# Performance work log

Measured on AMD Instinct MI355X. Metric: run time of the kernel, lower is better.

The kernel has to match this reference:

```python
import jax, jax.numpy as jnp
import numpy as np

H = 16  # heads
EPS_LN = 1e-5

def _ln(x, g, b):
    m = jnp.mean(x, axis=-1, keepdims=True)
    v = jnp.mean((x - m) ** 2, axis=-1, keepdims=True)
    return (x - m) / jnp.sqrt(v + EPS_LN) * g + b

def setup_inputs() -> dict:
    key = jax.random.key(0)
    B, L, d, mlp = 4, 4096, 1024, 4096
    ks = jax.random.split(key, 12)
    s = 0.02
    inp = {
        'x':   jax.random.normal(ks[0], (B, L, d), jnp.float32),
        'Wq':  jax.random.normal(ks[1], (d, d), jnp.float32) * s,
        'bq':  jnp.zeros((d,), jnp.float32),
        'gq':  jnp.ones((d,), jnp.float32),
        'betaq': jnp.zeros((d,), jnp.float32),
        'Wk':  jax.random.normal(ks[2], (d, d), jnp.float32) * s,
        'bk':  jnp.zeros((d,), jnp.float32),
        'gk':  jnp.ones((d,), jnp.float32),
        'betak': jnp.zeros((d,), jnp.float32),
        'Wv':  jax.random.normal(ks[3], (d, d), jnp.float32) * s,
        'bv':  jnp.zeros((d,), jnp.float32),
        'gv':  jnp.ones((d,), jnp.float32),
        'betav': jnp.zeros((d,), jnp.float32),
        'Wfq': jax.random.normal(ks[4], (d, d), jnp.float32) * s,
        'bfq': jnp.zeros((d,), jnp.float32),
        'Wfk': jax.random.normal(ks[5], (d, d), jnp.float32) * s,
        'bfk': jnp.zeros((d,), jnp.float32),
        'ga':  jnp.ones((d,), jnp.float32),
        'ba':  jnp.zeros((d,), jnp.float32),
        'W1':  jax.random.normal(ks[6], (d, mlp), jnp.float32) * s,
        'b1':  jnp.zeros((mlp,), jnp.float32),
        'W2':  jax.random.normal(ks[7], (mlp, d), jnp.float32) * s,
        'b2':  jnp.zeros((d,), jnp.float32),
    }
    return inp

def _fwd(x, Wq, bq, gq, betaq, Wk, bk, gk, betak, Wv, bv, gv, betav,
         Wfq, bfq, Wfk, bfk, ga, ba, W1, b1, W2, b2):
    B, L, d = x.shape
    D = d // H
    # Q/K/V projections + LayerNorm (dropout is eval-mode identity)
    Q = _ln(x @ Wq + bq, gq, betaq)                      # [B,L,d]
    Kc = _ln(x @ Wk + bk, gk, betak)                     # [B,L,d]
    Vc = _ln(x @ Wv + bv, gv, betav)                     # [B,L,d]
    # prepend zero token to K and V (add_zero_token=True)
    z = jnp.zeros((B, 1, d), x.dtype)
    K = jnp.concatenate([z, Kc], axis=1)                 # [B,Lk,d], Lk=L+1
    V = jnp.concatenate([z, Vc], axis=1)
    # kernel feature maps: tanh(Linear(.)) + 1
    phi_Q = jnp.tanh(Q @ Wfq + bfq) + 1.0
    phi_K = jnp.tanh(K @ Wfk + bfk) + 1.0
    split = lambda t: t.reshape(B, t.shape[1], H, D).transpose(0, 2, 1, 3)
    Qh, Kh, Vh = split(Q), split(K), split(V)            # [B,H,L(,k),D]
    pQ, pK = split(phi_Q), split(phi_K)
    # probe-softmax gating of phi_K
    q_probe = jnp.mean(Qh, axis=2) / jnp.sqrt(jnp.asarray(D, x.dtype))  # [B,H,D]
    score = jax.nn.softmax(jnp.einsum('bhd,bhkd->bhk', q_probe, Kh), axis=-1)  # [B,H,Lk]
    pKw = pK * score[..., None]                          # [B,H,Lk,D]
    # linear-attention fast path
    KV = jnp.einsum('bhkd,bhke->bhde', pKw, Vh)          # [B,H,D,D]
    Ksum = jnp.sum(pKw, axis=2)                          # [B,H,D]
    num = jnp.einsum('bhqd,bhde->bhqe', pQ, KV)          # [B,H,L,D]
    den = jnp.einsum('bhqd,bhd->bhq', pQ, Ksum)[..., None] + 1e-6
    out = num / den                                      # [B,H,L,D]
    out = out.transpose(0, 2, 1, 3).reshape(B, L, d)     # merge heads
    a = _ln(out, ga, ba)                                 # attn_norm
    # Residual MLP: a + Linear2(GELU(Linear1(a)))  (exact erf GELU)
    h = a + (jax.nn.gelu(a @ W1 + b1, approximate=False) @ W2 + b2)
    return h + x                                         # outer residual

def reference(x, Wq, bq, gq, betaq, Wk, bk, gk, betak, Wv, bv, gv, betav,
              Wfq, bfq, Wfk, bfk, ga, ba, W1, b1, W2, b2):
    return _fwd(x, Wq, bq, gq, betaq, Wk, bk, gk, betak, Wv, bv, gv, betav,
                Wfq, bfq, Wfk, bfk, ga, ba, W1, b1, W2, b2)
```

## Files before the change

### kernel.cpp

```cpp
#include <hip/hip_runtime.h>
#include <cstddef>
#include <cstdint>

static constexpr int Bc   = 4;
static constexpr int Lq   = 4096;
static constexpr int Dm   = 1024;
static constexpr int Dmlp = 4096;
static constexpr int Mrows = Bc * Lq;
static constexpr int Lk1   = Lq + 1;

typedef unsigned short u16;
typedef __bf16 bf16_t;
typedef bf16_t bf16x8 __attribute__((ext_vector_type(8)));
typedef float  f32x4  __attribute__((ext_vector_type(4)));

__device__ __forceinline__ u16 f2b(float f) {
    uint32_t u = __builtin_bit_cast(uint32_t, f);
    return (u16)((u + 0x7FFFu + ((u >> 16) & 1u)) >> 16);
}
__device__ __forceinline__ float b2f(u16 h) {
    uint32_t u = ((uint32_t)h) << 16;
    return __builtin_bit_cast(float, u);
}

#define GLL16(gsrc, ldst) \
    __builtin_amdgcn_global_load_lds( \
        (const __attribute__((address_space(1))) void*)(gsrc), \
        (__attribute__((address_space(3))) void*)(ldst), 16, 0, 0)

__global__ __launch_bounds__(256)
void zero_kernel(float* __restrict__ p, int n) {
    const int i = blockIdx.x * 256 + threadIdx.x;
    if (i < n) p[i] = 0.0f;
}

__global__ __launch_bounds__(256)
void cvt_bf16_kernel(const float* __restrict__ in, u16* __restrict__ outp, int n) {
    for (int i = (blockIdx.x * 256 + threadIdx.x) * 4; i < n; i += gridDim.x * 256 * 4) {
        float4 v = *(const float4*)&in[i];
        ushort4 o = { f2b(v.x), f2b(v.y), f2b(v.z), f2b(v.w) };
        *(ushort4*)&outp[i] = o;
    }
}

__global__ __launch_bounds__(256)
void transpose_bf16_kernel(const float* __restrict__ in, u16* __restrict__ outp,
                           int R, int C) {
    __shared__ float tile[64][65];
    const int r0 = blockIdx.y * 64, c0 = blockIdx.x * 64;
    const int t = threadIdx.x;
    const int lr = t >> 2, lc0 = (t & 3) * 16;
    #pragma unroll
    for (int j = 0; j < 4; ++j) {
        float4 v = *(const float4*)&in[(size_t)(r0 + lr) * C + c0 + lc0 + j * 4];
        tile[lr][lc0 + j * 4 + 0] = v.x;
        tile[lr][lc0 + j * 4 + 1] = v.y;
        tile[lr][lc0 + j * 4 + 2] = v.z;
        tile[lr][lc0 + j * 4 + 3] = v.w;
    }
    __syncthreads();
    const int oc = t >> 2, rr0 = (t & 3) * 16;
    union { u16 u[16]; uint4 v[2]; } pk;
    #pragma unroll
    for (int j = 0; j < 16; ++j) pk.u[j] = f2b(tile[rr0 + j][oc]);
    u16* po = &outp[(size_t)(c0 + oc) * R + r0 + rr0];
    *(uint4*)&po[0] = pk.v[0];
    *(uint4*)&po[8] = pk.v[1];
}

__global__ __launch_bounds__(256)
void kvt_cvt_kernel(const float* __restrict__ KV, u16* __restrict__ KVT) {
    const int bh = blockIdx.x;
    __shared__ float t[64][65];
    const int tid = threadIdx.x;
    const int r = tid >> 2, c0 = (tid & 3) * 16;
    const float* src = &KV[(size_t)bh * 4096];
    #pragma unroll
    for (int j = 0; j < 4; ++j) {
        float4 v = *(const float4*)&src[r * 64 + c0 + j * 4];
        t[r][c0 + j * 4 + 0] = v.x;
        t[r][c0 + j * 4 + 1] = v.y;
        t[r][c0 + j * 4 + 2] = v.z;
        t[r][c0 + j * 4 + 3] = v.w;
    }
    __syncthreads();
    const int e = tid >> 2, d0 = (tid & 3) * 16;
    union { u16 u[16]; uint4 v[2]; } pk;
    #pragma unroll
    for (int j = 0; j < 16; ++j) pk.u[j] = f2b(t[d0 + j][e]);
    u16* po = &KVT[(size_t)bh * 4096 + e * 64 + d0];
    *(uint4*)&po[0] = pk.v[0];
    *(uint4*)&po[8] = pk.v[1];
}

template<int ACT, bool RES, bool ACCUM, bool BIAS, bool OBF16>
__global__ __launch_bounds__(512, 1)
void mfma_gemm256(const u16* __restrict__ A, int ldA,
                  const u16* __restrict__ Bt, int ldB,
                  const float* __restrict__ bias,
                  void* __restrict__ Cout,
                  const u16* __restrict__ res1, const float* __restrict__ res2,
                  int M, int N, int K) {
    __shared__ u16 ldsA[4][8192];
    __shared__ u16 ldsB[4][8192];
    const int tid = threadIdx.x;
    const int l   = tid & 63;
    const int w   = tid >> 6;
    const int wm  = w >> 2;
    const int wn  = w & 3;
    const int l16 = l & 15, l4 = l >> 4;

    const int gx = N >> 8;
    int bid = blockIdx.x;
    bid = (bid & 7) * ((int)gridDim.x >> 3) + (bid >> 3);
    const int brow = (bid / gx) << 8;
    const int bcol = (bid % gx) << 8;

    const int srow = w * 16 + (l >> 2);
    const int skof = ((l & 3) ^ ((l >> 3) & 3)) << 3;
    const u16* gA = A  + (size_t)(brow + srow) * ldA + skof;
    const u16* gB = Bt + (size_t)(bcol + srow) * ldB + skof;
    const size_t gsA = (size_t)128 * ldA;
    const size_t gsB = (size_t)128 * ldB;
    const int ldst = w * 512 + l * 8;

    const int koff_rd = ((l4 ^ ((l16 >> 1) & 3)) << 3);
    const int aRdBase = (wm * 128 + l16) * 32 + koff_rd;
    const int bRdBase = (wn * 64  + l16) * 32 + koff_rd;

    f32x4 acc[8][4];
    const f32x4 zf = {0.f, 0.f, 0.f, 0.f};
    #pragma unroll
    for (int m = 0; m < 8; ++m)
        #pragma unroll
        for (int n = 0; n < 4; ++n) acc[m][n] = zf;

    auto stageA = [&](int slot, int kelem) {
        const u16* s = gA + (size_t)kelem;
        GLL16(s,       &ldsA[slot][ldst]);
        GLL16(s + gsA, &ldsA[slot][ldst + 4096]);
    };
    auto stageB = [&](int slot, int kelem) {
        const u16* s = gB + (size_t)kelem;
        GLL16(s,       &ldsB[slot][ldst]);
        GLL16(s + gsB, &ldsB[slot][ldst + 4096]);
    };

    const int T = K >> 5;
    stageA(0, 0);  stageB(0, 0);
    stageA(1, 32); stageB(1, 32);
    stageA(2, 64); stageB(2, 64);

    auto step = [&](int t, int waitsel, bool do_stage) {
        asm volatile("s_waitcnt lgkmcnt(0)" ::: "memory");
        if (waitsel == 0)      asm volatile("s_waitcnt vmcnt(8)" ::: "memory");
        else if (waitsel == 1) asm volatile("s_waitcnt vmcnt(4)" ::: "memory");
        else                   asm volatile("s_waitcnt vmcnt(0)" ::: "memory");
        asm volatile("s_barrier" ::: "memory");
        const int slot = t & 3;
        bf16x8 afr[4], bfr[4];
        #pragma unroll
        for (int n = 0; n < 4; ++n)
            bfr[n] = *(const bf16x8*)&ldsB[slot][bRdBase + n * 512];
        #pragma unroll
        for (int m = 0; m < 4; ++m)
            afr[m] = *(const bf16x8*)&ldsA[slot][aRdBase + m * 512];
        if (do_stage) stageA((t + 3) & 3, (t + 3) * 32);
        __builtin_amdgcn_s_setprio(1);
        #pragma unroll
        for (int m = 0; m < 4; ++m)
            #pragma unroll
            for (int n = 0; n < 4; ++n)
                acc[m][n] = __builtin_amdgcn_mfma_f32_16x16x32_bf16(
                    afr[m], bfr[n], acc[m][n], 0, 0, 0);
        __builtin_amdgcn_s_setprio(0);
        #pragma unroll
        for (int m = 0; m < 4; ++m)
            afr[m] = *(const bf16x8*)&ldsA[slot][aRdBase + (m + 4) * 512];
        if (do_stage) stageB((t + 3) & 3, (t + 3) * 32);
        __builtin_amdgcn_s_setprio(1);
        #pragma unroll
        for (int m = 0; m < 4; ++m)
            #pragma unroll
            for (int n = 0; n < 4; ++n)
                acc[m + 4][n] = __builtin_amdgcn_mfma_f32_16x16x32_bf16(
                    afr[m], bfr[n], acc[m + 4][n], 0, 0, 0);
        __builtin_amdgcn_s_setprio(0);
    };

    for (int t = 0; t < T - 2; ++t) step(t, 0, (t + 3) < T);
    step(T - 2, 1, false);
    step(T - 1, 2, false);

    float bvn[4];
    int coln[4];
    #pragma unroll
    for (int n = 0; n < 4; ++n) {
        coln[n] = bcol + wn * 64 + n * 16 + l16;
        bvn[n] = BIAS ? bias[coln[n]] : 0.f;
    }
    #pragma unroll
    for (int m = 0; m < 8; ++m) {
        #pragma unroll
        for (int q = 0; q < 4; ++q) {
            const size_t row = (size_t)brow + wm * 128 + m * 16 + l4 * 4 + q;
            #pragma unroll
            for (int n = 0; n < 4; ++n) {
                float v = acc[m][n][q] + bvn[n];
                if (ACT == 1) v = tanhf(v) + 1.0f;
                if (ACT == 2) v = 0.5f * v * (1.0f + erff(v * 0.70710678118654752f));
                const size_t idx = row * (size_t)N + coln[n];
                if (OBF16) {
                    ((u16*)Cout)[idx] = f2b(v);
                } else {
                    float* Cf = (float*)Cout;
                    if (ACCUM) v += Cf[idx];
                    if (RES)   v += b2f(res1[idx]) + res2[idx];
                    Cf[idx] = v;
                }
            }
        }
    }
}

__global__ __launch_bounds__(256)
void ln1024_bf16_kernel(const u16* __restrict__ in, u16* __restrict__ outp,
                        const float* __restrict__ g, const float* __restrict__ be) {
    const size_t base = (size_t)blockIdx.x * Dm;
    const int tid = threadIdx.x;
    ushort4 raw = *(const ushort4*)&in[base + tid * 4];
    float v0 = b2f(raw.x), v1 = b2f(raw.y), v2 = b2f(raw.z), v3 = b2f(raw.w);
    float s  = v0 + v1 + v2 + v3;
    float sq = v0 * v0 + v1 * v1 + v2 * v2 + v3 * v3;
    #pragma unroll
    for (int off = 32; off > 0; off >>= 1) {
        s  += __shfl_down(s,  off, 64);
        sq += __shfl_down(sq, off, 64);
    }
    __shared__ float rs[4], rq[4];
    const int lane = tid & 63, wv = tid >> 6;
    if (lane == 0) { rs[wv] = s; rq[wv] = sq; }
    __syncthreads();
    s  = rs[0] + rs[1] + rs[2] + rs[3];
    sq = rq[0] + rq[1] + rq[2] + rq[3];
    const float mean = s * (1.0f / 1024.0f);
    const float var  = sq * (1.0f / 1024.0f) - mean * mean;
    const float inv  = rsqrtf(var + 1e-5f);
    float4 gv = *(const float4*)&g[tid * 4];
    float4 bv = *(const float4*)&be[tid * 4];
    ushort4 o;
    o.x = f2b((v0 - mean) * inv * gv.x + bv.x);
    o.y = f2b((v1 - mean) * inv * gv.y + bv.y);
    o.z = f2b((v2 - mean) * inv * gv.z + bv.z);
    o.w = f2b((v3 - mean) * inv * gv.w + bv.w);
    *(ushort4*)&outp[base + tid * 4] = o;
}

__global__ __launch_bounds__(256)
void qprobe_kernel(const u16* __restrict__ Q, float* __restrict__ qp) {
    const int b = blockIdx.z;
    const int col = blockIdx.x * 256 + threadIdx.x;
    const int lchunk = Lq / 16;
    const int l0 = blockIdx.y * lchunk;
    const u16* p = Q + ((size_t)b * Lq + l0) * Dm + col;
    float s = 0.f;
    for (int l = 0; l < lchunk; ++l, p += Dm) s += b2f(*p);
    atomicAdd(&qp[b * Dm + col], s * (1.0f / (4096.0f * 8.0f)));
}

__global__ __launch_bounds__(256)
void logits_kernel(const u16* __restrict__ Kc, const float* __restrict__ qp,
                   float* __restrict__ score) {
    const int bh = blockIdx.y, b = bh >> 4, h = bh & 15;
    __shared__ float q[64];
    if (threadIdx.x < 64) q[threadIdx.x] = qp[b * Dm + h * 64 + threadIdx.x];
    __syncthreads();
    const int kr = blockIdx.x * 256 + threadIdx.x;
    const ushort4* krp = (const ushort4*)&Kc[((size_t)b * Lq + kr) * Dm + h * 64];
    float s = 0.f;
    #pragma unroll
    for (int i = 0; i < 16; ++i) {
        ushort4 v = krp[i];
        s += q[i * 4 + 0] * b2f(v.x) + q[i * 4 + 1] * b2f(v.y)
           + q[i * 4 + 2] * b2f(v.z) + q[i * 4 + 3] * b2f(v.w);
    }
    score[(size_t)bh * Lk1 + kr + 1] = s;
    if (blockIdx.x == 0 && threadIdx.x == 0) score[(size_t)bh * Lk1] = 0.f;
}

__global__ __launch_bounds__(256)
void softmax4097_kernel(float* __restrict__ sc) {
    __shared__ float buf[Lk1];
    __shared__ float red[8];
    const size_t base = (size_t)blockIdx.x * Lk1;
    const int tid = threadIdx.x;
    float mx = -1e30f;
    for (int i = tid; i < Lk1; i += 256) { float v = sc[base + i]; buf[i] = v; mx = fmaxf(mx, v); }
    #pragma unroll
    for (int off = 32; off > 0; off >>= 1) mx = fmaxf(mx, __shfl_down(mx, off, 64));
    const int lane = tid & 63, wv = tid >> 6;
    if (lane == 0) red[wv] = mx;
    __syncthreads();
    mx = fmaxf(fmaxf(red[0], red[1]), fmaxf(red[2], red[3]));
    float sum = 0.f;
    for (int i = tid; i < Lk1; i += 256) { float e = expf(buf[i] - mx); buf[i] = e; sum += e; }
    #pragma unroll
    for (int off = 32; off > 0; off >>= 1) sum += __shfl_down(sum, off, 64);
    if (lane == 0) red[4 + wv] = sum;
    __syncthreads();
    sum = red[4] + red[5] + red[6] + red[7];
    const float inv = 1.0f / sum;
    for (int i = tid; i < Lk1; i += 256) sc[base + i] = buf[i] * inv;
}

__global__ __launch_bounds__(256)
void kv_kernel(const u16* __restrict__ phiK, const u16* __restrict__ Vc,
               const float* __restrict__ sc, float* __restrict__ KV) {
    const int bh = blockIdx.y, b = bh >> 4, h = bh & 15;
    const int lchunk = Lq / 8;
    const int l0 = blockIdx.x * lchunk;
    __shared__ float pk[8][64];
    __shared__ float vv[8][64];
    const int i0 = (threadIdx.x >> 4) << 2;
    const int j0 = (threadIdx.x & 15) << 2;
    float acc[4][4] = {};
    for (int lb = l0; lb < l0 + lchunk; lb += 8) {
        #pragma unroll
        for (int q = 0; q < 2; ++q) {
            const int idx = threadIdx.x + q * 256;
            const int r = idx >> 6, c = idx & 63;
            const float scv = sc[(size_t)bh * Lk1 + lb + r + 1];
            const size_t off = ((size_t)b * Lq + lb + r) * Dm + h * 64 + c;
            pk[r][c] = b2f(phiK[off]) * scv;
            vv[r][c] = b2f(Vc[off]);
        }
        __syncthreads();
        #pragma unroll
        for (int r = 0; r < 8; ++r) {
            float ra[4], rb[4];
            #pragma unroll
            for (int i = 0; i < 4; ++i) ra[i] = pk[r][i0 + i];
            #pragma unroll
            for (int j = 0; j < 4; ++j) rb[j] = vv[r][j0 + j];
            #pragma unroll
            for (int i = 0; i < 4; ++i)
                #pragma unroll
                for (int j = 0; j < 4; ++j)
                    acc[i][j] = fmaf(ra[i], rb[j], acc[i][j]);
        }
        __syncthreads();
    }
    #pragma unroll
    for (int i = 0; i < 4; ++i)
        #pragma unroll
        for (int j = 0; j < 4; ++j)
            atomicAdd(&KV[((size_t)bh * 64 + i0 + i) * 64 + j0 + j], acc[i][j]);
}

__global__ __launch_bounds__(64)
void ksum_kernel(const u16* __restrict__ phiK, const float* __restrict__ sc,
                 const float* __restrict__ bfk, float* __restrict__ Ksum) {
    const int bh = blockIdx.y, b = bh >> 4, h = bh & 15;
    const int lchunk = Lq / 8;
    const int l0 = blockIdx.x * lchunk;
    const int dd = threadIdx.x;
    float s = 0.f;
    const u16* pp = &phiK[((size_t)b * Lq + l0) * Dm + h * 64 + dd];
    const float* sp = &sc[(size_t)bh * Lk1 + l0 + 1];
    for (int l = 0; l < lchunk; ++l, pp += Dm) s = fmaf(b2f(*pp), sp[l], s);
    if (blockIdx.x == 0) s += sc[(size_t)bh * Lk1] * (tanhf(bfk[h * 64 + dd]) + 1.0f);
    atomicAdd(&Ksum[bh * 64 + dd], s);
}

__global__ __launch_bounds__(256, 2)
void attnout_mfma_kernel(const u16* __restrict__ phiQ, const u16* __restrict__ KVT,
                         const float* __restrict__ Ksum, u16* __restrict__ outp) {
    __shared__ u16 pqs[256 * 64];
    __shared__ float kss[64];
    __shared__ float dns[256];
    const int bh = blockIdx.y, b = bh >> 4, h = bh & 15;
    const int l0 = blockIdx.x * 256;
    const int tid = threadIdx.x;
    const int l = tid & 63, w = tid >> 6;
    const int l16 = l & 15, l4 = l >> 4;

    bf16x8 bfr[4][2];
    {
        const u16* kb = KVT + (size_t)bh * 4096;
        #pragma unroll
        for (int n = 0; n < 4; ++n)
            #pragma unroll
            for (int kk = 0; kk < 2; ++kk)
                bfr[n][kk] = *(const bf16x8*)&kb[(n * 16 + l16) * 64 + kk * 32 + l4 * 8];
    }
    if (tid < 64) kss[tid] = Ksum[bh * 64 + tid];

    {
        const int rsub = tid >> 3;
        const int ssrc = ((tid & 7) ^ (rsub & 7)) * 8;
        u16* ldst = &pqs[(size_t)tid * 8];
        #pragma unroll
        for (int j = 0; j < 8; ++j) {
            const u16* g = phiQ + (((size_t)(b * Lq + l0 + j * 32 + rsub)) << 10)
                          + h * 64 + ssrc;
            GLL16(g, ldst + j * 2048);
        }
    }
    __syncthreads();

    {
        const int r7 = tid & 7;
        float s = 0.f;
        #pragma unroll
        for (int sl = 0; sl < 8; ++sl) {
            bf16x8 v = *(const bf16x8*)&pqs[tid * 64 + ((sl ^ r7) << 3)];
            #pragma unroll
            for (int j = 0; j < 8; ++j) s = fmaf(b2f(((u16*)&v)[j]), kss[sl * 8 + j], s);
        }
        dns[tid] = 1.0f / (s + 1e-6f);
    }

    f32x4 acc[4][4];
    const f32x4 zf = {0.f, 0.f, 0.f, 0.f};
    #pragma unroll
    for (int m = 0; m < 4; ++m)
        #pragma unroll
        for (int n = 0; n < 4; ++n) acc[m][n] = zf;
    #pragma unroll
    for (int kk = 0; kk < 2; ++kk) {
        bf16x8 afr[4];
        #pragma unroll
        for (int m = 0; m < 4; ++m) {
            const int row = w * 64 + m * 16 + l16;
            afr[m] = *(const bf16x8*)&pqs[row * 64 + (((kk * 4 + l4) ^ (row & 7)) << 3)];
        }
        #pragma unroll
        for (int m = 0; m < 4; ++m)
            #pragma unroll
            for (int n = 0; n < 4; ++n)
                acc[m][n] = __builtin_amdgcn_mfma_f32_16x16x32_bf16(
                    afr[m], bfr[n][kk], acc[m][n], 0, 0, 0);
    }
    __syncthreads();

    #pragma unroll
    for (int m = 0; m < 4; ++m) {
        #pragma unroll
        for (int q = 0; q < 4; ++q) {
            const int rl = w * 64 + m * 16 + l4 * 4 + q;
            const float dn = dns[rl];
            const size_t rowg = ((size_t)(b * Lq + l0 + rl)) << 10;
            #pragma unroll
            for (int n = 0; n < 4; ++n)
                outp[rowg + h * 64 + n * 16 + l16] = f2b(acc[m][n][q] * dn);
        }
    }
}

extern "C" void kernel_launch(void* const* d_in, const int* in_sizes, int n_in,
                              void* d_out, int out_size, void* d_ws, size_t ws_size,
                              hipStream_t stream) {
    const float* x     = (const float*)d_in[0];
    const float* Wq    = (const float*)d_in[1];
    const float* bq    = (const float*)d_in[2];
    const float* gq    = (const float*)d_in[3];
    const float* betaq = (const float*)d_in[4];
    const float* Wk    = (const float*)d_in[5];
    const float* bk    = (const float*)d_in[6];
    const float* gk    = (const float*)d_in[7];
    const float* betak = (const float*)d_in[8];
    const float* Wv    = (const float*)d_in[9];
    const float* bv    = (const float*)d_in[10];
    const float* gv    = (const float*)d_in[11];
    const float* betav = (const float*)d_in[12];
    const float* Wfq   = (const float*)d_in[13];
    const float* bfq   = (const float*)d_in[14];
    const float* Wfk   = (const float*)d_in[15];
    const float* bfk   = (const float*)d_in[16];
    const float* ga    = (const float*)d_in[17];
    const float* ba    = (const float*)d_in[18];
    const float* W1    = (const float*)d_in[19];
    const float* b1    = (const float*)d_in[20];
    const float* W2    = (const float*)d_in[21];
    const float* b2    = (const float*)d_in[22];
    float* outp = (float*)d_out;

    uint8_t* wsb = (uint8_t*)d_ws;
    size_t off = 0;
    auto alloc = [&](size_t bytes) { void* p = wsb + off; off += bytes; return p; };
    const size_t Md = (size_t)Mrows * Dm;
    u16* B0   = (u16*)alloc(Md * 2);
    u16* B1   = (u16*)alloc(Md * 2);
    u16* B2   = (u16*)alloc(Md * 2);
    u16* Wtq  = (u16*)alloc((size_t)Dm * Dm * 2);
    u16* Wtk  = (u16*)alloc((size_t)Dm * Dm * 2);
    u16* Wtv  = (u16*)alloc((size_t)Dm * Dm * 2);
    u16* Wtfq = (u16*)alloc((size_t)Dm * Dm * 2);
    u16* Wtfk = (u16*)alloc((size_t)Dm * Dm * 2);
    u16* Wt1  = (u16*)alloc((size_t)Dm * Dmlp * 2);
    u16* Wt2  = (u16*)alloc((size_t)Dm * Dmlp * 2);
    float* qp    = (float*)alloc(4096 * 4);
    float* KV    = (float*)alloc((size_t)64 * 64 * 64 * 4);
    float* Ksum  = (float*)alloc(4096 * 4);
    float* score = (float*)alloc((size_t)64 * Lk1 * 4);
    u16* KVT     = (u16*)alloc((size_t)64 * 64 * 64 * 2);
    u16* PK = (u16*)outp;
    u16* PQ = (u16*)outp + Md;

    const dim3 blk(256);
    const dim3 blk512(512);
    const dim3 gA(256);
    const dim3 gM(512);

    cvt_bf16_kernel<<<2048, blk, 0, stream>>>(x, B0, (int)Md);
    transpose_bf16_kernel<<<dim3(16, 16), blk, 0, stream>>>(Wq,  Wtq,  Dm, Dm);
    transpose_bf16_kernel<<<dim3(16, 16), blk, 0, stream>>>(Wk,  Wtk,  Dm, Dm);
    transpose_bf16_kernel<<<dim3(16, 16), blk, 0, stream>>>(Wv,  Wtv,  Dm, Dm);
    transpose_bf16_kernel<<<dim3(16, 16), blk, 0, stream>>>(Wfq, Wtfq, Dm, Dm);
    transpose_bf16_kernel<<<dim3(16, 16), blk, 0, stream>>>(Wfk, Wtfk, Dm, Dm);
    transpose_bf16_kernel<<<dim3(64, 16), blk, 0, stream>>>(W1,  Wt1,  Dm, Dmlp);
    transpose_bf16_kernel<<<dim3(16, 64), blk, 0, stream>>>(W2,  Wt2,  Dmlp, Dm);
    {
        const int nz = 4096 + 64 * 64 * 64 + 4096;
        zero_kernel<<<(nz + 255) / 256, blk, 0, stream>>>(qp, nz);
    }

    mfma_gemm256<0, false, false, true, true><<<gA, blk512, 0, stream>>>(
        B0, Dm, Wtq, Dm, bq, B1, nullptr, nullptr, Mrows, Dm, Dm);
    ln1024_bf16_kernel<<<Mrows, blk, 0, stream>>>(B1, B1, gq, betaq);
    mfma_gemm256<0, false, false, true, true><<<gA, blk512, 0, stream>>>(
        B0, Dm, Wtk, Dm, bk, B2, nullptr, nullptr, Mrows, Dm, Dm);
    ln1024_bf16_kernel<<<Mrows, blk, 0, stream>>>(B2, B2, gk, betak);

    qprobe_kernel<<<dim3(Dm / 256, 16, Bc), blk, 0, stream>>>(B1, qp);
    logits_kernel<<<dim3(Lq / 256, 64), blk, 0, stream>>>(B2, qp, score);
    softmax4097_kernel<<<64, blk, 0, stream>>>(score);

    mfma_gemm256<1, false, false, true, true><<<gA, blk512, 0, stream>>>(
        B2, Dm, Wtfk, Dm, bfk, PK, nullptr, nullptr, Mrows, Dm, Dm);
    mfma_gemm256<1, false, false, true, true><<<gA, blk512, 0, stream>>>(
        B1, Dm, Wtfq, Dm, bfq, PQ, nullptr, nullptr, Mrows, Dm, Dm);

    mfma_gemm256<0, false, false, true, true><<<gA, blk512, 0, stream>>>(
        B0, Dm, Wtv, Dm, bv, B1, nullptr, nullptr, Mrows, Dm, Dm);
    ln1024_bf16_kernel<<<Mrows, blk, 0, stream>>>(B1, B1, gv, betav);

    kv_kernel<<<dim3(8, 64), blk, 0, stream>>>(PK, B1, score, KV);
    ksum_kernel<<<dim3(8, 64), dim3(64), 0, stream>>>(PK, score, bfk, Ksum);
    kvt_cvt_kernel<<<64, blk, 0, stream>>>(KV, KVT);

    attnout_mfma_kernel<<<dim3(Lq / 256, 64), blk, 0, stream>>>(PQ, KVT, Ksum, B2);
    ln1024_bf16_kernel<<<Mrows, blk, 0, stream>>>(B2, B2, ga, ba);

    u16* H1 = B0;
    for (int c = 0; c < 2; ++c) {
        mfma_gemm256<2, false, false, true, true><<<gM, blk512, 0, stream>>>(
            B2, Dm, Wt1 + (size_t)c * 2048 * Dm, Dm, b1 + c * 2048,
            H1, nullptr, nullptr, Mrows, 2048, Dm);
        if (c == 0) {
            mfma_gemm256<0, false, false, true, false><<<gA, blk512, 0, stream>>>(
                H1, 2048, Wt2 + (size_t)c * 2048, Dmlp, b2,
                outp, nullptr, nullptr, Mrows, Dm, 2048);
        } else {
            mfma_gemm256<0, true, true, false, false><<<gA, blk512, 0, stream>>>(
                H1, 2048, Wt2 + (size_t)c * 2048, Dmlp, nullptr,
                outp, B2, x, Mrows, Dm, 2048);
        }
    }
}
```

Baseline: 782.5 us.

## Fuse prep launches, merge Q/K projection GEMMs, fold Ksum into KV kernel

Several setup launches are collapsed into one prep_kernel: the x-to-bf16 conversion, the seven weight transposes, the zeroing and a concatenated Q/K bias. The Q and K projections become a single N=2048 GEMM whose epilogue routes columns to two output buffers through new Cout2/nSplit/ldc arguments. The K-sum reduction now runs inside kv_kernel, which also loads its inputs with paired 2-element loads. The aim is to cut launch overhead and the separate ksum pass over phiK, and to give the GPU more blocks per GEMM. The merged GEMM assumes the Wtk buffer sits directly after Wtq in memory.

```diff
diff --git a/kernel.cpp b/kernel.cpp
--- a/kernel.cpp
+++ b/kernel.cpp
@@ -28,26 +28,11 @@
         (const __attribute__((address_space(1))) void*)(gsrc), \
         (__attribute__((address_space(3))) void*)(ldst), 16, 0, 0)
 
-__global__ __launch_bounds__(256)
-void zero_kernel(float* __restrict__ p, int n) {
-    const int i = blockIdx.x * 256 + threadIdx.x;
-    if (i < n) p[i] = 0.0f;
-}
-
-__global__ __launch_bounds__(256)
-void cvt_bf16_kernel(const float* __restrict__ in, u16* __restrict__ outp, int n) {
-    for (int i = (blockIdx.x * 256 + threadIdx.x) * 4; i < n; i += gridDim.x * 256 * 4) {
-        float4 v = *(const float4*)&in[i];
-        ushort4 o = { f2b(v.x), f2b(v.y), f2b(v.z), f2b(v.w) };
-        *(ushort4*)&outp[i] = o;
-    }
-}
-
-__global__ __launch_bounds__(256)
-void transpose_bf16_kernel(const float* __restrict__ in, u16* __restrict__ outp,
-                           int R, int C) {
+__device__ __forceinline__
+void transpose_tile(const float* __restrict__ in, u16* __restrict__ outp,
+                    int R, int C, int tx, int ty) {
     __shared__ float tile[64][65];
-    const int r0 = blockIdx.y * 64, c0 = blockIdx.x * 64;
+    const int r0 = ty * 64, c0 = tx * 64;
     const int t = threadIdx.x;
     const int lr = t >> 2, lc0 = (t & 3) * 16;
     #pragma unroll
@@ -66,6 +51,61 @@
     u16* po = &outp[(size_t)(c0 + oc) * R + r0 + rr0];
     *(uint4*)&po[0] = pk.v[0];
     *(uint4*)&po[8] = pk.v[1];
+}
+
+__global__ __launch_bounds__(256)
+void prep_kernel(const float* __restrict__ x, u16* __restrict__ xb,
+                 const float* __restrict__ Wq, const float* __restrict__ Wk,
+                 const float* __restrict__ Wv, const float* __restrict__ Wfq,
+                 const float* __restrict__ Wfk, const float* __restrict__ W1,
+                 const float* __restrict__ W2,
+                 u16* __restrict__ Wtq, u16* __restrict__ Wtk,
+                 u16* __restrict__ Wtv, u16* __restrict__ Wtfq,
+                 u16* __restrict__ Wtfk, u16* __restrict__ Wt1,
+                 u16* __restrict__ Wt2,
+                 const float* __restrict__ bq, const float* __restrict__ bk,
+                 float* __restrict__ bqk,
+                 float* __restrict__ zp, int nz) {
+    int bid = blockIdx.x;
+    if (bid < 2048) {
+        const int n = Mrows * Dm;
+        for (int i = (bid * 256 + threadIdx.x) * 4; i < n; i += 2048 * 256 * 4) {
+            float4 v = *(const float4*)&x[i];
+            ushort4 o = { f2b(v.x), f2b(v.y), f2b(v.z), f2b(v.w) };
+            *(ushort4*)&xb[i] = o;
+        }
+        return;
+    }
+    bid -= 2048;
+    if (bid < 3328) {
+        const float* src; u16* dst; int R, C, tx, ty;
+        if (bid < 1280) {
+            const int wsel = bid >> 8, rem = bid & 255;
+            if      (wsel == 0) { src = Wq;  dst = Wtq;  }
+            else if (wsel == 1) { src = Wk;  dst = Wtk;  }
+            else if (wsel == 2) { src = Wv;  dst = Wtv;  }
+            else if (wsel == 3) { src = Wfq; dst = Wtfq; }
+            else                { src = Wfk; dst = Wtfk; }
+            R = 1024; C = 1024; tx = rem & 15; ty = rem >> 4;
+        } else if (bid < 2304) {
+            const int rem = bid - 1280;
+            src = W1; dst = Wt1; R = 1024; C = 4096; tx = rem & 63; ty = rem >> 6;
+        } else {
+            const int rem = bid - 2304;
+            src = W2; dst = Wt2; R = 4096; C = 1024; tx = rem & 15; ty = rem >> 4;
+        }
+        transpose_tile(src, dst, R, C, tx, ty);
+        return;
+    }
+    bid -= 3328;
+    if (bid < 1056) {
+        const int i = bid * 256 + threadIdx.x;
+        if (i < nz) zp[i] = 0.0f;
+        return;
+    }
+    bid -= 1056;
+    const int i = bid * 256 + threadIdx.x;
+    bqk[i] = (i < 1024) ? bq[i] : bk[i - 1024];
 }
 
 __global__ __launch_bounds__(256)
@@ -98,7 +138,8 @@
 void mfma_gemm256(const u16* __restrict__ A, int ldA,
                   const u16* __restrict__ Bt, int ldB,
                   const float* __restrict__ bias,
-                  void* __restrict__ Cout,
+                  void* __restrict__ Cout, void* __restrict__ Cout2,
+                  int nSplit, int ldc,
                   const u16* __restrict__ res1, const float* __restrict__ res2,
                   int M, int N, int K) {
     __shared__ u16 ldsA[4][8192];
@@ -192,12 +233,17 @@
     step(T - 2, 1, false);
     step(T - 1, 2, false);
 
+    const bool hiC = (bcol >= nSplit);
+    u16*   Co16 = (u16*)(hiC ? Cout2 : Cout);
+    float* Co32 = (float*)Cout;
+    const int bcolE = bcol - (hiC ? nSplit : 0);
     float bvn[4];
-    int coln[4];
+    int colE[4];
     #pragma unroll
     for (int n = 0; n < 4; ++n) {
-        coln[n] = bcol + wn * 64 + n * 16 + l16;
-        bvn[n] = BIAS ? bias[coln[n]] : 0.f;
+        const int cg = bcol + wn * 64 + n * 16 + l16;
+        colE[n] = bcolE + wn * 64 + n * 16 + l16;
+        bvn[n] = BIAS ? bias[cg] : 0.f;
     }
     #pragma unroll
     for (int m = 0; m < 8; ++m) {
@@ -209,14 +255,13 @@
                 float v = acc[m][n][q] + bvn[n];
                 if (ACT == 1) v = tanhf(v) + 1.0f;
                 if (ACT == 2) v = 0.5f * v * (1.0f + erff(v * 0.70710678118654752f));
-                const size_t idx = row * (size_t)N + coln[n];
+                const size_t idx = row * (size_t)ldc + colE[n];
                 if (OBF16) {
-                    ((u16*)Cout)[idx] = f2b(v);
+                    Co16[idx] = f2b(v);
                 } else {
-                    float* Cf = (float*)Cout;
-                    if (ACCUM) v += Cf[idx];
+                    if (ACCUM) v += Co32[idx];
                     if (RES)   v += b2f(res1[idx]) + res2[idx];
-                    Cf[idx] = v;
+                    Co32[idx] = v;
                 }
             }
         }
@@ -315,25 +360,31 @@
 
 __global__ __launch_bounds__(256)
 void kv_kernel(const u16* __restrict__ phiK, const u16* __restrict__ Vc,
-               const float* __restrict__ sc, float* __restrict__ KV) {
+               const float* __restrict__ sc, const float* __restrict__ bfk,
+               float* __restrict__ KV, float* __restrict__ Ksum) {
     const int bh = blockIdx.y, b = bh >> 4, h = bh & 15;
     const int lchunk = Lq / 8;
     const int l0 = blockIdx.x * lchunk;
     __shared__ float pk[8][64];
     __shared__ float vv[8][64];
+    __shared__ float red[8][64];
     const int i0 = (threadIdx.x >> 4) << 2;
     const int j0 = (threadIdx.x & 15) << 2;
+    const int srr = threadIdx.x >> 5;
+    const int scc = (threadIdx.x & 31) << 1;
     float acc[4][4] = {};
+    float ks0 = 0.f, ks1 = 0.f;
     for (int lb = l0; lb < l0 + lchunk; lb += 8) {
-        #pragma unroll
-        for (int q = 0; q < 2; ++q) {
-            const int idx = threadIdx.x + q * 256;
-            const int r = idx >> 6, c = idx & 63;
-            const float scv = sc[(size_t)bh * Lk1 + lb + r + 1];
-            const size_t off = ((size_t)b * Lq + lb + r) * Dm + h * 64 + c;
-            pk[r][c] = b2f(phiK[off]) * scv;
-            vv[r][c] = b2f(Vc[off]);
-        }
+        const float scv = sc[(size_t)bh * Lk1 + lb + srr + 1];
+        const size_t off = ((size_t)b * Lq + lb + srr) * Dm + h * 64 + scc;
+        ushort2 pv = *(const ushort2*)&phiK[off];
+        ushort2 vb = *(const ushort2*)&Vc[off];
+        const float p0 = b2f(pv.x) * scv, p1 = b2f(pv.y) * scv;
+        pk[srr][scc]     = p0;
+        pk[srr][scc + 1] = p1;
+        vv[srr][scc]     = b2f(vb.x);
+        vv[srr][scc + 1] = b2f(vb.y);
+        ks0 += p0; ks1 += p1;
         __syncthreads();
         #pragma unroll
         for (int r = 0; r < 8; ++r) {
@@ -350,26 +401,22 @@
         }
         __syncthreads();
     }
+    red[srr][scc] = ks0;
+    red[srr][scc + 1] = ks1;
+    __syncthreads();
+    if (threadIdx.x < 64) {
+        float s = 0.f;
+        #pragma unroll
+        for (int r = 0; r < 8; ++r) s += red[r][threadIdx.x];
+        if (blockIdx.x == 0)
+            s += sc[(size_t)bh * Lk1] * (tanhf(bfk[h * 64 + threadIdx.x]) + 1.0f);
+        atomicAdd(&Ksum[bh * 64 + threadIdx.x], s);
+    }
     #pragma unroll
     for (int i = 0; i < 4; ++i)
         #pragma unroll
         for (int j = 0; j < 4; ++j)
             atomicAdd(&KV[((size_t)bh * 64 + i0 + i) * 64 + j0 + j], acc[i][j]);
-}
-
-__global__ __launch_bounds__(64)
-void ksum_kernel(const u16* __restrict__ phiK, const float* __restrict__ sc,
-                 const float* __restrict__ bfk, float* __restrict__ Ksum) {
-    const int bh = blockIdx.y, b = bh >> 4, h = bh & 15;
-    const int lchunk = Lq / 8;
-    const int l0 = blockIdx.x * lchunk;
-    const int dd = threadIdx.x;
-    float s = 0.f;
-    const u16* pp = &phiK[((size_t)b * Lq + l0) * Dm + h * 64 + dd];
-    const float* sp = &sc[(size_t)bh * Lk1 + l0 + 1];
-    for (int l = 0; l < lchunk; ++l, pp += Dm) s = fmaf(b2f(*pp), sp[l], s);
-    if (blockIdx.x == 0) s += sc[(size_t)bh * Lk1] * (tanhf(bfk[h * 64 + dd]) + 1.0f);
-    atomicAdd(&Ksum[bh * 64 + dd], s);
 }
 
 __global__ __launch_bounds__(256, 2)
@@ -504,32 +551,26 @@
     float* Ksum  = (float*)alloc(4096 * 4);
     float* score = (float*)alloc((size_t)64 * Lk1 * 4);
     u16* KVT     = (u16*)alloc((size_t)64 * 64 * 64 * 2);
+    float* bqk   = (float*)alloc(2048 * 4);
     u16* PK = (u16*)outp;
     u16* PQ = (u16*)outp + Md;
 
     const dim3 blk(256);
     const dim3 blk512(512);
     const dim3 gA(256);
+    const dim3 gQK(512);
     const dim3 gM(512);
 
-    cvt_bf16_kernel<<<2048, blk, 0, stream>>>(x, B0, (int)Md);
-    transpose_bf16_kernel<<<dim3(16, 16), blk, 0, stream>>>(Wq,  Wtq,  Dm, Dm);
-    transpose_bf16_kernel<<<dim3(16, 16), blk, 0, stream>>>(Wk,  Wtk,  Dm, Dm);
-    transpose_bf16_kernel<<<dim3(16, 16), blk, 0, stream>>>(Wv,  Wtv,  Dm, Dm);
-    transpose_bf16_kernel<<<dim3(16, 16), blk, 0, stream>>>(Wfq, Wtfq, Dm, Dm);
-    transpose_bf16_kernel<<<dim3(16, 16), blk, 0, stream>>>(Wfk, Wtfk, Dm, Dm);
-    transpose_bf16_kernel<<<dim3(64, 16), blk, 0, stream>>>(W1,  Wt1,  Dm, Dmlp);
-    transpose_bf16_kernel<<<dim3(16, 64), blk, 0, stream>>>(W2,  Wt2,  Dmlp, Dm);
-    {
-        const int nz = 4096 + 64 * 64 * 64 + 4096;
-        zero_kernel<<<(nz + 255) / 256, blk, 0, stream>>>(qp, nz);
-    }
-
-    mfma_gemm256<0, false, false, true, true><<<gA, blk512, 0, stream>>>(
-        B0, Dm, Wtq, Dm, bq, B1, nullptr, nullptr, Mrows, Dm, Dm);
+    const int nz = 4096 + 64 * 64 * 64 + 4096;
+    prep_kernel<<<6440, blk, 0, stream>>>(
+        x, B0, Wq, Wk, Wv, Wfq, Wfk, W1, W2,
+        Wtq, Wtk, Wtv, Wtfq, Wtfk, Wt1, Wt2,
+        bq, bk, bqk, qp, nz);
+
+    mfma_gemm256<0, false, false, true, true><<<gQK, blk512, 0, stream>>>(
+        B0, Dm, Wtq, Dm, bqk, B1, B2, 1024, 1024, nullptr, nullptr,
+        Mrows, 2048, Dm);
     ln1024_bf16_kernel<<<Mrows, blk, 0, stream>>>(B1, B1, gq, betaq);
-    mfma_gemm256<0, false, false, true, true><<<gA, blk512, 0, stream>>>(
-        B0, Dm, Wtk, Dm, bk, B2, nullptr, nullptr, Mrows, Dm, Dm);
     ln1024_bf16_kernel<<<Mrows, blk, 0, stream>>>(B2, B2, gk, betak);
 
     qprobe_kernel<<<dim3(Dm / 256, 16, Bc), blk, 0, stream>>>(B1, qp);
@@ -537,16 +578,18 @@
     softmax4097_kernel<<<64, blk, 0, stream>>>(score);
 
     mfma_gemm256<1, false, false, true, true><<<gA, blk512, 0, stream>>>(
-        B2, Dm, Wtfk, Dm, bfk, PK, nullptr, nullptr, Mrows, Dm, Dm);
+        B2, Dm, Wtfk, Dm, bfk, PK, PK, Dm, Dm, nullptr, nullptr,
+        Mrows, Dm, Dm);
     mfma_gemm256<1, false, false, true, true><<<gA, blk512, 0, stream>>>(
-        B1, Dm, Wtfq, Dm, bfq, PQ, nullptr, nullptr, Mrows, Dm, Dm);
+        B1, Dm, Wtfq, Dm, bfq, PQ, PQ, Dm, Dm, nullptr, nullptr,
+        Mrows, Dm, Dm);
 
     mfma_gemm256<0, false, false, true, true><<<gA, blk512, 0, stream>>>(
-        B0, Dm, Wtv, Dm, bv, B1, nullptr, nullptr, Mrows, Dm, Dm);
+        B0, Dm, Wtv, Dm, bv, B1, B1, Dm, Dm, nullptr, nullptr,
+        Mrows, Dm, Dm);
     ln1024_bf16_kernel<<<Mrows, blk, 0, stream>>>(B1, B1, gv, betav);
 
-    kv_kernel<<<dim3(8, 64), blk, 0, stream>>>(PK, B1, score, KV);
-    ksum_kernel<<<dim3(8, 64), dim3(64), 0, stream>>>(PK, score, bfk, Ksum);
+    kv_kernel<<<dim3(8, 64), blk, 0, stream>>>(PK, B1, score, bfk, KV, Ksum);
     kvt_cvt_kernel<<<64, blk, 0, stream>>>(KV, KVT);
 
     attnout_mfma_kernel<<<dim3(Lq / 256, 64), blk, 0, stream>>>(PQ, KVT, Ksum, B2);
@@ -556,15 +599,15 @@
     for (int c = 0; c < 2; ++c) {
         mfma_gemm256<2, false, false, true, true><<<gM, blk512, 0, stream>>>(
             B2, Dm, Wt1 + (size_t)c * 2048 * Dm, Dm, b1 + c * 2048,
-            H1, nullptr, nullptr, Mrows, 2048, Dm);
+            H1, H1, 2048, 2048, nullptr, nullptr, Mrows, 2048, Dm);
         if (c == 0) {
             mfma_gemm256<0, false, false, true, false><<<gA, blk512, 0, stream>>>(
                 H1, 2048, Wt2 + (size_t)c * 2048, Dmlp, b2,
-                outp, nullptr, nullptr, Mrows, Dm, 2048);
+                outp, outp, Dm, Dm, nullptr, nullptr, Mrows, Dm, 2048);
         } else {
             mfma_gemm256<0, true, true, false, false><<<gA, blk512, 0, stream>>>(
                 H1, 2048, Wt2 + (size_t)c * 2048, Dmlp, nullptr,
-                outp, B2, x, Mrows, Dm, 2048);
-        }
-    }
-}
+                outp, outp, Dm, Dm, B2, x, Mrows, Dm, 2048);
+        }
+    }
+}
```

Result: faster. 766.0 us (median of 2 runs) (-2.1%).
